# Kernel optimization log

Measured on AMD Instinct MI355X. Metric: run time of the kernel, lower is better.

Reference implementation:

```python
import jax, jax.numpy as jnp
import numpy as np

OUT, IN = 4096, 4096
B, S = 4, 2048


def _quantize(w):
    # replicate torch LinearAffine8bit.__init__ affine quantization
    min_val, max_val = jnp.min(w), jnp.max(w)
    scale = (max_val - min_val) / 255.0
    zp = 255.0 - max_val / scale
    zp = jnp.clip(zp, 0.0, 255.0)
    zp = jnp.round(zp)
    q = jnp.round(jnp.clip(zp + w / scale, 0.0, 255.0)).astype(jnp.int32)
    return q, scale, zp


def setup_inputs() -> dict:
    key = jax.random.key(0)
    kx, kw, kb = jax.random.split(key, 3)
    x = jax.random.normal(kx, (B, S, IN), dtype=jnp.float32)
    w_fp = jax.random.normal(kw, (OUT, IN), dtype=jnp.float32) * 0.02
    bias = jax.random.normal(kb, (OUT,), dtype=jnp.float32) * 0.01
    qweight, scale, zero_point = _quantize(w_fp)
    return {"x": x, "qweight": qweight, "scale": scale,
            "zero_point": zero_point, "bias": bias}


def reference(x, qweight, scale, zero_point, bias):
    # F.linear(x, scale * (qweight - zero_point), bias)
    w = scale * (qweight.astype(x.dtype) - zero_point)  # [OUT, IN] dequant
    return jnp.einsum('bsi,oi->bso', x, w) + bias
```

## Files before the change

### kernel.cpp

```cpp
#include <hip/hip_runtime.h>
#include <hip/hip_bf16.h>
#include <stdint.h>

#define M_DIM 8192
#define N_DIM 4096
#define K_DIM 4096

typedef __attribute__((ext_vector_type(4))) int i32x4;
typedef __attribute__((ext_vector_type(8))) __bf16 bf16x8;
typedef __attribute__((ext_vector_type(4))) float f32x4;
typedef __attribute__((ext_vector_type(8))) unsigned short ushort8;

__device__ __forceinline__ unsigned short f2bf(float f) {
  union { float f; uint32_t u; } v; v.f = f;
  uint32_t u = v.u;
  return (unsigned short)((u + 0x7FFFu + ((u >> 16) & 1u)) >> 16);
}

__device__ __forceinline__ void gload_lds16(const void* g, void* l) {
  __builtin_amdgcn_global_load_lds((const __attribute__((address_space(1))) void*)g,
                                   (__attribute__((address_space(3))) void*)l,
                                   16, 0, 0);
}

#define RAW_BAR() asm volatile("s_barrier" ::: "memory")
#define VMW(n) asm volatile("s_waitcnt vmcnt(" #n ")" ::: "memory")
#define LGKM0()                                        \
  do {                                                 \
    asm volatile("s_waitcnt lgkmcnt(0)" ::: "memory"); \
    __builtin_amdgcn_sched_barrier(0);                 \
  } while (0)
#define SBAR0() __builtin_amdgcn_sched_barrier(0)

#define WN4 ((long long)N_DIM * K_DIM / 4)
#define WBLOCKS 2048

__global__ __launch_bounds__(256) void prepack_kernel(
    const float* __restrict__ x, const int* __restrict__ q,
    const float* __restrict__ scale, const float* __restrict__ zp,
    char* __restrict__ xq, char* __restrict__ wq,
    float* __restrict__ rsw, float* __restrict__ corr) {
  const int b = blockIdx.x;
  const int t = threadIdx.x;
  if (b < M_DIM) {
    const int row = b;
    const float4* xr = (const float4*)(x + (size_t)row * K_DIM);
    float4 v[4];
    float mx = 0.f;
    #pragma unroll
    for (int i = 0; i < 4; ++i) {
      v[i] = xr[i * 256 + t];
      mx = fmaxf(mx, fmaxf(fmaxf(fabsf(v[i].x), fabsf(v[i].y)),
                           fmaxf(fabsf(v[i].z), fabsf(v[i].w))));
    }
    __shared__ float redm[4], reds[4];
    #pragma unroll
    for (int off = 32; off; off >>= 1) mx = fmaxf(mx, __shfl_xor(mx, off));
    if ((t & 63) == 0) redm[t >> 6] = mx;
    __syncthreads();
    mx = fmaxf(fmaxf(redm[0], redm[1]), fmaxf(redm[2], redm[3]));
    mx = fmaxf(mx, 1e-20f);
    const float inv = 127.f / mx;
    float sum = 0.f;
    int* xqo = (int*)xq + (size_t)row * (K_DIM / 4);
    #pragma unroll
    for (int i = 0; i < 4; ++i) {
      sum += v[i].x + v[i].y + v[i].z + v[i].w;
      int q0 = (int)rintf(v[i].x * inv), q1 = (int)rintf(v[i].y * inv);
      int q2 = (int)rintf(v[i].z * inv), q3 = (int)rintf(v[i].w * inv);
      xqo[i * 256 + t] = (q0 & 255) | ((q1 & 255) << 8) | ((q2 & 255) << 16) | (q3 << 24);
    }
    #pragma unroll
    for (int off = 32; off; off >>= 1) sum += __shfl_xor(sum, off);
    if ((t & 63) == 0) reds[t >> 6] = sum;
    __syncthreads();
    if (t == 0) {
      const float sw = scale[0], zw = zp[0];
      rsw[row] = (mx / 127.f) * sw;
      corr[row] = sw * (128.f - zw) * (reds[0] + reds[1] + reds[2] + reds[3]);
    }
  } else {
    long long i = (long long)(b - M_DIM) * 256 + t;
    const long long stride = (long long)WBLOCKS * 256;
    int* wo = (int*)wq;
    for (; i < WN4; i += stride) {
      const int4 a = ((const int4*)q)[i];
      wo[i] = ((a.x - 128) & 255) | (((a.y - 128) & 255) << 8) |
              (((a.z - 128) & 255) << 16) | ((a.w - 128) << 24);
    }
  }
}

#define NTILE (K_DIM / 64)
#define BUFB 32768

__global__ __launch_bounds__(512, 2) void gemm256_i8_kernel(
    const char* __restrict__ xq, const char* __restrict__ wq,
    const float* __restrict__ rsw, const float* __restrict__ corr,
    const float* __restrict__ bias, float* __restrict__ out) {
  __shared__ char lds[4 * BUFB];

  const int t = threadIdx.x;
  const int lane = t & 63;
  const int wid = t >> 6;
  const int wr = wid >> 2;
  const int wc = wid & 3;
  const int fr = lane & 15, fq = lane >> 4;

  const int bid = blockIdx.x;
  const int swz = ((bid & 7) << 6) | (bid >> 3);
  const int bx = swz & 15;
  const int by = swz >> 4;
  const int brow = by * 256, bcol = bx * 256;

  const int gsrc = (t & 3) ^ ((t >> 3) & 3);
  const char* gAs = xq + (size_t)(brow + (t >> 2)) * K_DIM + gsrc * 16;
  const char* gBs = wq + (size_t)(bcol + (t >> 2)) * K_DIM + gsrc * 16;

  const int gsel16 = (fq ^ ((fr >> 1) & 3)) * 16;
  const int arow = (wr * 128 + fr) * 64;
  const int brow_o = 16384 + (wc * 64 + fr) * 64;

  i32x4 af[8], bfv[2][4];
  i32x4 acc[8][4] = {};

  #define LD_A(b, m) (*(const i32x4*)(lds + (b) * BUFB + arow + (m) * 1024 + gsel16))
  #define LD_B(b, n) (*(const i32x4*)(lds + (b) * BUFB + brow_o + (n) * 1024 + gsel16))

  #define RD_H1(b, p)                                                          \
    { af[0] = LD_A(b, 0); af[1] = LD_A(b, 1); af[2] = LD_A(b, 2);              \
      af[3] = LD_A(b, 3);                                                      \
      bfv[p][0] = LD_B(b, 0); bfv[p][1] = LD_B(b, 1);                          \
      bfv[p][2] = LD_B(b, 2); bfv[p][3] = LD_B(b, 3); }
  #define RD_H2(b)                                                             \
    { af[4] = LD_A(b, 4); af[5] = LD_A(b, 5); af[6] = LD_A(b, 6);              \
      af[7] = LD_A(b, 7); }

  #define STG(isB, h, tile, b)                                                 \
    do {                                                                       \
      char* l_ = lds + (b) * BUFB + (isB) * 16384 + (h) * 8192 + t * 16;       \
      const char* g_ = ((isB) ? gBs : gAs) + (size_t)(h) * 128 * K_DIM +       \
                       (size_t)(tile) * 64;                                    \
      gload_lds16(g_, l_);                                                     \
    } while (0)

  #define MMQ(MS, p)                                                           \
    __builtin_amdgcn_s_setprio(1);                                             \
    _Pragma("unroll")                                                          \
    for (int m = 0; m < 4; ++m) {                                              \
      _Pragma("unroll")                                                        \
      for (int n = 0; n < 4; ++n)                                              \
        acc[MS + m][n] = __builtin_amdgcn_mfma_i32_16x16x64_i8(                \
            af[MS + m], bfv[p][n], acc[MS + m][n], 0, 0, 0);                   \
    }                                                                          \
    __builtin_amdgcn_s_setprio(0);                                             \
    SBAR0();

  #define PH_A(b, p, Xp3, B3, WT_)                                             \
    LGKM0(); RD_H2(b) MMQ(0, p)                                                \
    STG(1, 0, Xp3, B3); STG(1, 1, Xp3, B3); WT_; RAW_BAR();
  #define PH_B(bN, p, np, Xp3, B3)                                             \
    LGKM0(); RD_H1(bN, np) MMQ(4, p)                                           \
    STG(0, 0, Xp3, B3); STG(0, 1, Xp3, B3); RAW_BAR();

  #define TILE_FULL(b, bN, B3, p, np, Xp3)                                     \
    PH_A(b, p, Xp3, B3, VMW(6))                                                \
    PH_B(bN, p, np, Xp3, B3)

  STG(1, 0, 0, 0); STG(1, 1, 0, 0); STG(0, 0, 0, 0); STG(0, 1, 0, 0);
  STG(1, 0, 1, 1); STG(1, 1, 1, 1); STG(0, 0, 1, 1); STG(0, 1, 1, 1);
  STG(1, 0, 2, 2); STG(1, 1, 2, 2); STG(0, 0, 2, 2); STG(0, 1, 2, 2);
  VMW(8);
  RAW_BAR();
  RD_H1(0, 0)

  for (int jj = 0; jj < 15; ++jj) {
    const int X0 = 4 * jj;
    TILE_FULL(0, 1, 3, 0, 1, X0 + 3)
    TILE_FULL(1, 2, 0, 1, 0, X0 + 4)
    TILE_FULL(2, 3, 1, 0, 1, X0 + 5)
    TILE_FULL(3, 0, 2, 1, 0, X0 + 6)
  }
  TILE_FULL(0, 1, 3, 0, 1, 63)
  PH_A(1, 1, 0, 0, VMW(4))
  PH_B(2, 1, 0, 0, 0)
  LGKM0(); RD_H2(2) MMQ(0, 0) VMW(0); RAW_BAR();
  LGKM0(); RD_H1(3, 1) MMQ(4, 0) RAW_BAR();
  LGKM0(); RD_H2(3) MMQ(0, 1)
  LGKM0(); MMQ(4, 1)

  #undef LD_A
  #undef LD_B
  #undef RD_H1
  #undef RD_H2
  #undef STG
  #undef MMQ
  #undef PH_A
  #undef PH_B
  #undef TILE_FULL

  float bv[4];
  #pragma unroll
  for (int n = 0; n < 4; ++n) bv[n] = bias[bcol + wc * 64 + n * 16 + fr];
  #pragma unroll
  for (int m = 0; m < 8; ++m) {
    #pragma unroll
    for (int j = 0; j < 4; ++j) {
      const int row = brow + wr * 128 + m * 16 + fq * 4 + j;
      const float rs_ = rsw[row], co_ = corr[row];
      #pragma unroll
      for (int n = 0; n < 4; ++n) {
        const int col = bcol + wc * 64 + n * 16 + fr;
        out[(size_t)row * N_DIM + col] = (float)acc[m][n][j] * rs_ + co_ + bv[n];
      }
    }
  }
}

__global__ __launch_bounds__(256) void gemm_fallback_kernel(
    const float* __restrict__ x, const int* __restrict__ qw,
    const float* __restrict__ scale, const float* __restrict__ zp,
    const float* __restrict__ bias, float* __restrict__ out) {
  __shared__ unsigned short lds_a[128 * 32];
  __shared__ unsigned short lds_b[128 * 32];
  const int t = threadIdx.x;
  const int lane = t & 63;
  const int wid = t >> 6;
  const int wr = wid >> 1, wc = wid & 1;
  const int fr = lane & 15, fq = lane >> 4;
  const int nwg = gridDim.x;
  const int cpx = nwg >> 3;
  const int bid = blockIdx.x;
  const int swz = (bid & 7) * cpx + (bid >> 3);
  const int bx = swz & 31, by = swz >> 5;
  const int brow = by * 128, bcol = bx * 128;
  const int r0 = t >> 2, c8 = (t & 3) * 8;
  f32x4 acc[4][4] = {};
  const float ss = scale[0], zs = zp[0];
  for (int kk = 0; kk < K_DIM; kk += 32) {
    ushort8 ua[2], ub[2];
    #pragma unroll
    for (int i = 0; i < 2; ++i) {
      const float* gp = x + (size_t)(brow + i * 64 + r0) * K_DIM + kk + c8;
      float4 v0 = *(const float4*)gp;
      float4 v1 = *(const float4*)(gp + 4);
      ua[i][0] = f2bf(v0.x); ua[i][1] = f2bf(v0.y); ua[i][2] = f2bf(v0.z); ua[i][3] = f2bf(v0.w);
      ua[i][4] = f2bf(v1.x); ua[i][5] = f2bf(v1.y); ua[i][6] = f2bf(v1.z); ua[i][7] = f2bf(v1.w);
      const int* qp = qw + (size_t)(bcol + i * 64 + r0) * K_DIM + kk + c8;
      int4 q0 = *(const int4*)qp;
      int4 q1 = *(const int4*)(qp + 4);
      ub[i][0] = f2bf(ss * ((float)q0.x - zs)); ub[i][1] = f2bf(ss * ((float)q0.y - zs));
      ub[i][2] = f2bf(ss * ((float)q0.z - zs)); ub[i][3] = f2bf(ss * ((float)q0.w - zs));
      ub[i][4] = f2bf(ss * ((float)q1.x - zs)); ub[i][5] = f2bf(ss * ((float)q1.y - zs));
      ub[i][6] = f2bf(ss * ((float)q1.z - zs)); ub[i][7] = f2bf(ss * ((float)q1.w - zs));
    }
    __syncthreads();
    #pragma unroll
    for (int i = 0; i < 2; ++i) {
      *(ushort8*)(lds_a + ((size_t)i * 256 + t) * 8) = ua[i];
      *(ushort8*)(lds_b + ((size_t)i * 256 + t) * 8) = ub[i];
    }
    __syncthreads();
    bf16x8 af[4], bfr[4];
    #pragma unroll
    for (int m = 0; m < 4; ++m)
      af[m] = *(const bf16x8*)(lds_a + (wr * 64 + m * 16 + fr) * 32 + fq * 8);
    #pragma unroll
    for (int n = 0; n < 4; ++n)
      bfr[n] = *(const bf16x8*)(lds_b + (wc * 64 + n * 16 + fr) * 32 + fq * 8);
    #pragma unroll
    for (int m = 0; m < 4; ++m)
      #pragma unroll
      for (int n = 0; n < 4; ++n)
        acc[m][n] = __builtin_amdgcn_mfma_f32_16x16x32_bf16(af[m], bfr[n], acc[m][n], 0, 0, 0);
  }
  #pragma unroll
  for (int n = 0; n < 4; ++n) {
    const int col = bcol + wc * 64 + n * 16 + fr;
    const float bvv = bias[col];
    #pragma unroll
    for (int m = 0; m < 4; ++m) {
      const int rowb = brow + wr * 64 + m * 16 + fq * 4;
      #pragma unroll
      for (int j = 0; j < 4; ++j)
        out[(size_t)(rowb + j) * N_DIM + col] = acc[m][n][j] + bvv;
    }
  }
}

extern "C" void kernel_launch(void* const* d_in, const int* in_sizes, int n_in,
                              void* d_out, int out_size, void* d_ws, size_t ws_size,
                              hipStream_t stream) {
  const float* x = (const float*)d_in[0];
  const int* qw = (const int*)d_in[1];
  const float* scale = (const float*)d_in[2];
  const float* zp = (const float*)d_in[3];
  const float* bias = (const float*)d_in[4];
  float* out = (float*)d_out;

  const size_t xq_bytes = (size_t)M_DIM * K_DIM;
  const size_t wq_bytes = (size_t)N_DIM * K_DIM;
  const size_t rsw_bytes = (size_t)M_DIM * 4;
  const size_t need = xq_bytes + wq_bytes + 2 * rsw_bytes;

  if (ws_size >= need) {
    char* xq = (char*)d_ws;
    char* wq = (char*)d_ws + xq_bytes;
    float* rsw = (float*)((char*)d_ws + xq_bytes + wq_bytes);
    float* corr = rsw + M_DIM;
    prepack_kernel<<<M_DIM + WBLOCKS, 256, 0, stream>>>(x, qw, scale, zp, xq, wq, rsw, corr);
    const int grid = (M_DIM / 256) * (N_DIM / 256);
    gemm256_i8_kernel<<<grid, 512, 0, stream>>>(xq, wq, rsw, corr, bias, out);
  } else {
    const int grid = (M_DIM / 128) * (N_DIM / 128);
    gemm_fallback_kernel<<<grid, 256, 0, stream>>>(x, qw, scale, zp, bias, out);
  }
}
```

Before: 178.5 us.

## Split int8 GEMM main loop into four quarter-phases with finer LDS/MFMA interleave

Restructures the software-pipelined int8 MFMA main loop from two half-phases per K-tile into four quarter-phases, each issuing 8 MFMAs interleaved with one global-to-LDS stage and a partial LDS fragment read. The B fragment buffer shrinks from double-buffered to single, which lowers register pressure, and the loop is written as a single counted loop instead of a manually unrolled four-tile body. The aim is to hide LDS read latency behind smaller MFMA groups. In exchange it adds twice as many barriers per tile, which may cost synchronisation overhead.

After: 181.2 us. No clear change (+1.6%).

```diff
diff --git a/kernel.cpp b/kernel.cpp
--- a/kernel.cpp
+++ b/kernel.cpp
@@ -121,18 +121,17 @@
   const int arow = (wr * 128 + fr) * 64;
   const int brow_o = 16384 + (wc * 64 + fr) * 64;
 
-  i32x4 af[8], bfv[2][4];
+  i32x4 af[8], bfv[4];
   i32x4 acc[8][4] = {};
 
   #define LD_A(b, m) (*(const i32x4*)(lds + (b) * BUFB + arow + (m) * 1024 + gsel16))
   #define LD_B(b, n) (*(const i32x4*)(lds + (b) * BUFB + brow_o + (n) * 1024 + gsel16))
 
-  #define RD_H1(b, p)                                                          \
+  #define RD_Q1(b)                                                             \
     { af[0] = LD_A(b, 0); af[1] = LD_A(b, 1); af[2] = LD_A(b, 2);              \
-      af[3] = LD_A(b, 3);                                                      \
-      bfv[p][0] = LD_B(b, 0); bfv[p][1] = LD_B(b, 1);                          \
-      bfv[p][2] = LD_B(b, 2); bfv[p][3] = LD_B(b, 3); }
-  #define RD_H2(b)                                                             \
+      af[3] = LD_A(b, 3); bfv[0] = LD_B(b, 0); bfv[1] = LD_B(b, 1); }
+  #define RD_Q2(b) { bfv[2] = LD_B(b, 2); bfv[3] = LD_B(b, 3); }
+  #define RD_Q3(b)                                                             \
     { af[4] = LD_A(b, 4); af[5] = LD_A(b, 5); af[6] = LD_A(b, 6);              \
       af[7] = LD_A(b, 7); }
 
@@ -144,60 +143,55 @@
       gload_lds16(g_, l_);                                                     \
     } while (0)
 
-  #define MMQ(MS, p)                                                           \
+  #define MMQ(MS, NS)                                                          \
     __builtin_amdgcn_s_setprio(1);                                             \
     _Pragma("unroll")                                                          \
     for (int m = 0; m < 4; ++m) {                                              \
       _Pragma("unroll")                                                        \
-      for (int n = 0; n < 4; ++n)                                              \
-        acc[MS + m][n] = __builtin_amdgcn_mfma_i32_16x16x64_i8(                \
-            af[MS + m], bfv[p][n], acc[MS + m][n], 0, 0, 0);                   \
+      for (int n = 0; n < 2; ++n)                                              \
+        acc[MS + m][NS + n] = __builtin_amdgcn_mfma_i32_16x16x64_i8(           \
+            af[MS + m], bfv[NS + n], acc[MS + m][NS + n], 0, 0, 0);            \
     }                                                                          \
     __builtin_amdgcn_s_setprio(0);                                             \
     SBAR0();
-
-  #define PH_A(b, p, Xp3, B3, WT_)                                             \
-    LGKM0(); RD_H2(b) MMQ(0, p)                                                \
-    STG(1, 0, Xp3, B3); STG(1, 1, Xp3, B3); WT_; RAW_BAR();
-  #define PH_B(bN, p, np, Xp3, B3)                                             \
-    LGKM0(); RD_H1(bN, np) MMQ(4, p)                                           \
-    STG(0, 0, Xp3, B3); STG(0, 1, Xp3, B3); RAW_BAR();
-
-  #define TILE_FULL(b, bN, B3, p, np, Xp3)                                     \
-    PH_A(b, p, Xp3, B3, VMW(6))                                                \
-    PH_B(bN, p, np, Xp3, B3)
 
   STG(1, 0, 0, 0); STG(1, 1, 0, 0); STG(0, 0, 0, 0); STG(0, 1, 0, 0);
   STG(1, 0, 1, 1); STG(1, 1, 1, 1); STG(0, 0, 1, 1); STG(0, 1, 1, 1);
   STG(1, 0, 2, 2); STG(1, 1, 2, 2); STG(0, 0, 2, 2); STG(0, 1, 2, 2);
   VMW(8);
   RAW_BAR();
-  RD_H1(0, 0)
-
-  for (int jj = 0; jj < 15; ++jj) {
-    const int X0 = 4 * jj;
-    TILE_FULL(0, 1, 3, 0, 1, X0 + 3)
-    TILE_FULL(1, 2, 0, 1, 0, X0 + 4)
-    TILE_FULL(2, 3, 1, 0, 1, X0 + 5)
-    TILE_FULL(3, 0, 2, 1, 0, X0 + 6)
-  }
-  TILE_FULL(0, 1, 3, 0, 1, 63)
-  PH_A(1, 1, 0, 0, VMW(4))
-  PH_B(2, 1, 0, 0, 0)
-  LGKM0(); RD_H2(2) MMQ(0, 0) VMW(0); RAW_BAR();
-  LGKM0(); RD_H1(3, 1) MMQ(4, 0) RAW_BAR();
-  LGKM0(); RD_H2(3) MMQ(0, 1)
-  LGKM0(); MMQ(4, 1)
+  RD_Q1(0)
+
+  for (int X = 0; X <= 60; ++X) {
+    const int b  = X & 3;
+    const int bN = (X + 1) & 3;
+    const int B3 = (X + 3) & 3;
+    const int T3 = X + 3;
+    LGKM0(); MMQ(0, 0) STG(1, 0, T3, B3); RD_Q2(b) RAW_BAR();
+    LGKM0(); MMQ(0, 2) STG(1, 1, T3, B3); RD_Q3(b) RAW_BAR();
+    LGKM0(); MMQ(4, 0) STG(0, 0, T3, B3); VMW(7); RAW_BAR();
+    MMQ(4, 2) STG(0, 1, T3, B3); RD_Q1(bN) RAW_BAR();
+  }
+  LGKM0(); MMQ(0, 0) RD_Q2(1) RAW_BAR();
+  LGKM0(); MMQ(0, 2) RD_Q3(1) RAW_BAR();
+  LGKM0(); MMQ(4, 0) VMW(4); RAW_BAR();
+  MMQ(4, 2) RD_Q1(2) RAW_BAR();
+  LGKM0(); MMQ(0, 0) RD_Q2(2) RAW_BAR();
+  LGKM0(); MMQ(0, 2) RD_Q3(2) RAW_BAR();
+  LGKM0(); MMQ(4, 0) VMW(0); RAW_BAR();
+  MMQ(4, 2) RD_Q1(3) RAW_BAR();
+  LGKM0(); MMQ(0, 0) RD_Q2(3) RAW_BAR();
+  LGKM0(); MMQ(0, 2) RD_Q3(3) RAW_BAR();
+  LGKM0(); MMQ(4, 0) RAW_BAR();
+  MMQ(4, 2)
 
   #undef LD_A
   #undef LD_B
-  #undef RD_H1
-  #undef RD_H2
+  #undef RD_Q1
+  #undef RD_Q2
+  #undef RD_Q3
   #undef STG
   #undef MMQ
-  #undef PH_A
-  #undef PH_B
-  #undef TILE_FULL
 
   float bv[4];
   #pragma unroll
```
